# Kernel tuning notes

Measured on AMD Instinct MI355X. Metric: run time of the kernel, lower is better.

## Reference

```python
import jax, jax.numpy as jnp
import numpy as np

EMBED_DIM = 768
NUM_HEADS = 12


def setup_inputs() -> dict:
    key = jax.random.key(0)
    k_x, k_w1, k_b1, k_w2, k_b2 = jax.random.split(key, 5)
    B, S, D = 4, 2048, EMBED_DIM
    s1 = 1.0 / np.sqrt(D)
    return {
        "x": jax.random.normal(k_x, (B, S, D), dtype=jnp.float32),
        "W1": jax.random.uniform(k_w1, (D, 3 * D), jnp.float32, -s1, s1),  # proj1 weight (in,out)
        "b1": jax.random.uniform(k_b1, (3 * D,), jnp.float32, -s1, s1),
        "W2": jax.random.uniform(k_w2, (D, D), jnp.float32, -s1, s1),  # proj2 weight (in,out)
        "b2": jax.random.uniform(k_b2, (D,), jnp.float32, -s1, s1),
    }


def reference(x, W1, b1, W2, b2):
    B, S, D = x.shape
    H = NUM_HEADS
    h = D // H
    qkv = x @ W1 + b1                       # [B,S,3D]
    qkv = qkv.reshape(B, S, H, 3 * h).transpose(0, 2, 1, 3)  # [B,H,S,3h]
    # chunk order in the original: K, Q, V
    K = qkv[..., :h]
    Q = qkv[..., h:2 * h]
    V = qkv[..., 2 * h:]
    # NOTE: original code computes Q @ V^T (not Q @ K^T) -- reproduced faithfully
    scores = jnp.einsum("bhqd,bhkd->bhqk", Q, V) / jnp.sqrt(jnp.float32(h))
    att = jax.nn.softmax(scores, axis=-1)
    out = jnp.einsum("bhqk,bhkd->bhqd", att, V)  # [B,H,S,h]
    out = out.transpose(0, 2, 1, 3).reshape(B, S, D)
    return out @ W2 + b2
```

## Files before the change

### kernel.cpp

```cpp
#include <hip/hip_runtime.h>
#include <hip/hip_bf16.h>
#include <math.h>


#define SEQ   2048
#define DIM   768
#define NHEAD 12
#define HDIM  64
#define BATCH 4

#define QSCALE 0.1803368801111244f

typedef __attribute__((ext_vector_type(8))) short s16x8;
typedef __attribute__((ext_vector_type(4))) float f32x4;

#if __has_builtin(__builtin_amdgcn_exp2f)
#define EXP2F(x) __builtin_amdgcn_exp2f(x)
#else
#define EXP2F(x) exp2f(x)
#endif

__device__ __forceinline__ unsigned short f2bf(float f) {
    union { float f; unsigned int u; } v; v.f = f;
    unsigned int r = v.u + 0x7fffu + ((v.u >> 16) & 1u);
    return (unsigned short)(r >> 16);
}

__device__ __forceinline__ unsigned int cvt_pk_bf16(float a, float b) {
    unsigned int r;
    asm("v_cvt_pk_bf16_f32 %0, %1, %2" : "=v"(r) : "v"(a), "v"(b));
    return r;
}

__device__ __forceinline__ void gload_lds16(const void* g, void* l) {
    __builtin_amdgcn_global_load_lds(
        (const __attribute__((address_space(1))) unsigned int*)g,
        (__attribute__((address_space(3))) unsigned int*)l, 16, 0, 0);
}

__global__ __launch_bounds__(256) void cvt_all(
    const float* __restrict__ x, const float* __restrict__ W1,
    const float* __restrict__ W2, unsigned short* __restrict__ xb,
    unsigned short* __restrict__ W1bt, unsigned short* __restrict__ W2bt)
{
    __shared__ float T[32][33];
    const int id = blockIdx.x;

    if (id >= 1728) {
        const size_t i4 = ((size_t)(id - 1728) * 256 + threadIdx.x) * 4;
        float4 v = *(const float4*)&x[i4];
        ushort4 o;
        o.x = f2bf(v.x); o.y = f2bf(v.y); o.z = f2bf(v.z); o.w = f2bf(v.w);
        *(ushort4*)&xb[i4] = o;
        return;
    }

    const float* W;
    unsigned short* out;
    int n0, k0, src_ld, c0;
    if (id < 1152) {
        W = W1; out = W1bt; src_ld = 2304;
        n0 = (id % 48) * 32; k0 = (id / 48) * 32;
        c0 = (n0 >> 7) * 192 + 64 + (n0 & 127);
    } else {
        const int id2 = id - 1152;
        W = W2; out = W2bt; src_ld = DIM;
        n0 = (id2 % 24) * 32; k0 = (id2 / 24) * 32;
        c0 = n0;
    }
    const int tc = threadIdx.x & 31, tr = threadIdx.x >> 5;
    #pragma unroll
    for (int i = 0; i < 4; ++i)
        T[tr + i * 8][tc] = W[(size_t)(k0 + tr + i * 8) * src_ld + c0 + tc];
    __syncthreads();
    #pragma unroll
    for (int i = 0; i < 4; ++i)
        out[(size_t)(n0 + tr + i * 8) * DIM + k0 + tc] = f2bf(T[tc][tr + i * 8]);
}

__device__ __forceinline__ void gemm128_loop_dbuf(
    const unsigned short* __restrict__ A, const unsigned short* __restrict__ B,
    unsigned short* L, int m0, int n0, f32x4 acc[4][4])
{
    const int tid  = threadIdx.x;
    const int wave = tid >> 6;
    const int lane = tid & 63;
    const int quad = lane >> 4;
    const int lcol = lane & 15;
    const int wm = wave >> 1, wn = wave & 1;

    const int sr = lane >> 2;
    const int sp = lane & 3;
    const int sc = sp ^ ((sr >> 1) & 3);

    const int aswz = ((quad ^ ((lcol >> 1) & 3)) << 4);

    s16x8 ra[2], rb[2];
    #pragma unroll
    for (int s = 0; s < 2; ++s) {
        const int r0 = wave * 32 + s * 16;
        ra[s] = *(const s16x8*)&A[(size_t)(m0 + r0 + sr) * DIM + sc * 8];
        rb[s] = *(const s16x8*)&B[(size_t)(n0 + r0 + sr) * DIM + sc * 8];
    }
    #pragma unroll
    for (int s = 0; s < 2; ++s) {
        const int r0 = wave * 32 + s * 16;
        *(s16x8*)((char*)(L + r0 * 32) + lane * 16) = ra[s];
        *(s16x8*)((char*)(L + 8192 + r0 * 32) + lane * 16) = rb[s];
    }
    __syncthreads();

    int cur = 0;
    for (int k0 = 0; k0 < DIM; k0 += 32) {
        const bool more = (k0 + 32 < DIM);
        if (more) {
            #pragma unroll
            for (int s = 0; s < 2; ++s) {
                const int r0 = wave * 32 + s * 16;
                ra[s] = *(const s16x8*)&A[(size_t)(m0 + r0 + sr) * DIM + k0 + 32 + sc * 8];
                rb[s] = *(const s16x8*)&B[(size_t)(n0 + r0 + sr) * DIM + k0 + 32 + sc * 8];
            }
            __builtin_amdgcn_sched_barrier(0);
        }

        const unsigned short* AsC = L + cur * 4096;
        const unsigned short* BsC = L + 8192 + cur * 4096;

        s16x8 af[4], bf[4];
        #pragma unroll
        for (int mt = 0; mt < 4; ++mt) {
            const int row = wm * 64 + mt * 16 + lcol;
            af[mt] = *(const s16x8*)((const char*)AsC + row * 64 + aswz);
        }
        #pragma unroll
        for (int nt = 0; nt < 4; ++nt) {
            const int row = wn * 64 + nt * 16 + lcol;
            bf[nt] = *(const s16x8*)((const char*)BsC + row * 64 + aswz);
        }
        #pragma unroll
        for (int mt = 0; mt < 4; ++mt)
            #pragma unroll
            for (int nt = 0; nt < 4; ++nt)
                acc[mt][nt] = __builtin_amdgcn_mfma_f32_16x16x32_bf16(
                    af[mt], bf[nt], acc[mt][nt], 0, 0, 0);

        if (more) {
            const int nb = cur ^ 1;
            #pragma unroll
            for (int s = 0; s < 2; ++s) {
                const int r0 = wave * 32 + s * 16;
                *(s16x8*)((char*)(L + nb * 4096 + r0 * 32) + lane * 16) = ra[s];
                *(s16x8*)((char*)(L + 8192 + nb * 4096 + r0 * 32) + lane * 16) = rb[s];
            }
        }
        __syncthreads();
        cur ^= 1;
    }
}

__global__ __launch_bounds__(256) void qkv_gemm_bf16(
    const unsigned short* __restrict__ xb, const unsigned short* __restrict__ W1bt,
    const float* __restrict__ b1, unsigned short* __restrict__ Qb,
    unsigned short* __restrict__ Vr, unsigned short* __restrict__ Vt)
{
    __shared__ unsigned short LDSBUF[16384];
    f32x4 acc[4][4] = {};
    const int id  = blockIdx.y * 12 + blockIdx.x;
    const int swz = (id & 7) * 96 + (id >> 3);
    const int m0 = (swz / 12) * 128, n0 = (swz % 12) * 128;
    gemm128_loop_dbuf(xb, W1bt, LDSBUF, m0, n0, acc);

    const int tid  = threadIdx.x;
    const int wave = tid >> 6, lane = tid & 63;
    const int quad = lane >> 4, lcol = lane & 15;
    const int wm = wave >> 1, wn = wave & 1;

    const int colblock = n0 + wn * 64;
    const int head = colblock >> 7;
    const int cc0  = colblock & 127;
    const int isQ  = (cc0 == 0);
    const float scale = isQ ? QSCALE : 1.0f;
    unsigned short* dst = isQ ? Qb : Vr;

    float bias[4];
    #pragma unroll
    for (int nt = 0; nt < 4; ++nt)
        bias[nt] = b1[head * 192 + 64 + cc0 + nt * 16 + lcol];

    unsigned short* Wst = LDSBUF + wave * 2048;

    #pragma unroll
    for (int half = 0; half < 2; ++half) {
        #pragma unroll
        for (int mh = 0; mh < 2; ++mh) {
            const int mt = half * 2 + mh;
            #pragma unroll
            for (int nt = 0; nt < 4; ++nt)
                #pragma unroll
                for (int r = 0; r < 4; ++r) {
                    const float v = (acc[mt][nt][r] + bias[nt]) * scale;
                    Wst[(mh * 16 + quad * 4 + r) * 64 + nt * 16 + lcol] = f2bf(v);
                }
        }
        __syncthreads();
        #pragma unroll
        for (int p = 0; p < 4; ++p) {
            const int lr = p * 8 + (lane >> 3);
            const int c8 = (lane & 7) * 8;
            s16x8 v = *(const s16x8*)&Wst[lr * 64 + c8];
            const int m  = m0 + wm * 64 + half * 32 + lr;
            const int bb = m >> 11;
            const int s  = m & 2047;
            const int bhh = bb * NHEAD + head;
            *(s16x8*)&dst[((size_t)bhh * SEQ + s) * HDIM + c8] = v;
        }
        __syncthreads();
    }

    if (!isQ) {
        #pragma unroll
        for (int nt = 0; nt < 4; ++nt) {
            const int d = nt * 16 + lcol;
            #pragma unroll
            for (int mt = 0; mt < 4; ++mt) {
                const int m0r = m0 + wm * 64 + mt * 16 + quad * 4;
                const int bb  = m0r >> 11;
                const int s0  = m0r & 2047;
                const int bhh = bb * NHEAD + head;
                ushort4 o;
                o.x = f2bf(acc[mt][nt][0] + bias[nt]);
                o.y = f2bf(acc[mt][nt][1] + bias[nt]);
                o.z = f2bf(acc[mt][nt][2] + bias[nt]);
                o.w = f2bf(acc[mt][nt][3] + bias[nt]);
                *(ushort4*)&Vt[((size_t)bhh * HDIM + d) * SEQ + s0] = o;
            }
        }
    }
}

__global__ __launch_bounds__(256) void attn_mfma(
    const unsigned short* __restrict__ Qb, const unsigned short* __restrict__ Vr,
    const unsigned short* __restrict__ Vt, unsigned short* __restrict__ Yb)
{
    __shared__ unsigned short VrS[2][64 * 64];
    __shared__ unsigned short VtS[2][64 * 64];
    __shared__ unsigned short Ps[4][32 * 72];

    const int bh = blockIdx.x;
    const int b  = bh / NHEAD;
    const int hh = bh % NHEAD;
    const int q0 = blockIdx.y * 128;

    const int tid  = threadIdx.x;
    const int wave = tid >> 6;
    const int lane = tid & 63;
    const int quad = lane >> 4;
    const int lcol = lane & 15;

    s16x8 qa[2][2];
    #pragma unroll
    for (int mt = 0; mt < 2; ++mt)
        #pragma unroll
        for (int kk = 0; kk < 2; ++kk)
            qa[mt][kk] = *(const s16x8*)&Qb[((size_t)bh * SEQ + q0 + wave * 32 + mt * 16 + lcol) * HDIM
                                            + kk * 32 + quad * 8];

    s16x8 ones;
    #pragma unroll
    for (int i = 0; i < 8; ++i) ones[i] = (short)0x3F80;

    f32x4 oacc[2][4] = {};
    f32x4 lsum[2] = {};

    const int srow = lane >> 3;
    const int schk = (lane & 7) ^ srow;

    s16x8 rv[2], rt[2];
    #pragma unroll
    for (int s = 0; s < 2; ++s) {
        const int r0 = wave * 16 + s * 8;
        rv[s] = *(const s16x8*)&Vr[((size_t)bh * SEQ + r0 + srow) * HDIM + schk * 8];
        rt[s] = *(const s16x8*)&Vt[((size_t)bh * HDIM + r0 + srow) * SEQ + schk * 8];
    }
    #pragma unroll
    for (int s = 0; s < 2; ++s) {
        const int r0 = wave * 16 + s * 8;
        *(s16x8*)((char*)&VrS[0][r0 * 64] + lane * 16) = rv[s];
        *(s16x8*)((char*)&VtS[0][r0 * 64] + lane * 16) = rt[s];
    }
    __syncthreads();

    int cur = 0;
    for (int k0 = 0; k0 < SEQ; k0 += 64) {
        const bool more = (k0 + 64 < SEQ);
        if (more) {
            #pragma unroll
            for (int s = 0; s < 2; ++s) {
                const int r0 = wave * 16 + s * 8;
                rv[s] = *(const s16x8*)&Vr[((size_t)bh * SEQ + k0 + 64 + r0 + srow) * HDIM + schk * 8];
                rt[s] = *(const s16x8*)&Vt[((size_t)bh * HDIM + r0 + srow) * SEQ + k0 + 64 + schk * 8];
            }
            __builtin_amdgcn_sched_barrier(0);
        }

        const unsigned short* VrC = &VrS[cur][0];
        const unsigned short* VtC = &VtS[cur][0];

        f32x4 sT[4][2] = {};
        #pragma unroll
        for (int kk = 0; kk < 2; ++kk) {
            s16x8 af[4];
            #pragma unroll
            for (int kt = 0; kt < 4; ++kt) {
                const int r = kt * 16 + lcol;
                const int c = kk * 4 + quad;
                af[kt] = *(const s16x8*)((const char*)VrC + r * 128 + ((c ^ (r & 7)) << 4));
            }
            #pragma unroll
            for (int kt = 0; kt < 4; ++kt)
                #pragma unroll
                for (int mt = 0; mt < 2; ++mt)
                    sT[kt][mt] = __builtin_amdgcn_mfma_f32_16x16x32_bf16(
                        af[kt], qa[mt][kk], sT[kt][mt], 0, 0, 0);
        }

        #pragma unroll
        for (int kt = 0; kt < 4; ++kt)
            #pragma unroll
            for (int mt = 0; mt < 2; ++mt) {
                const float p0 = EXP2F(sT[kt][mt][0]);
                const float p1 = EXP2F(sT[kt][mt][1]);
                const float p2 = EXP2F(sT[kt][mt][2]);
                const float p3 = EXP2F(sT[kt][mt][3]);
                uint2 w;
                w.x = cvt_pk_bf16(p0, p1);
                w.y = cvt_pk_bf16(p2, p3);
                *(uint2*)&Ps[wave][(mt * 16 + lcol) * 72 + kt * 16 + quad * 4] = w;
            }

        #pragma unroll
        for (int kk = 0; kk < 2; ++kk) {
            s16x8 pa[2];
            #pragma unroll
            for (int mt = 0; mt < 2; ++mt)
                pa[mt] = *(const s16x8*)&Ps[wave][(mt * 16 + lcol) * 72 + kk * 32 + quad * 8];
            #pragma unroll
            for (int mt = 0; mt < 2; ++mt)
                lsum[mt] = __builtin_amdgcn_mfma_f32_16x16x32_bf16(
                    pa[mt], ones, lsum[mt], 0, 0, 0);
            #pragma unroll
            for (int dt = 0; dt < 4; ++dt) {
                const int r = dt * 16 + lcol;
                const int c = kk * 4 + quad;
                s16x8 vb = *(const s16x8*)((const char*)VtC + r * 128 + ((c ^ (r & 7)) << 4));
                #pragma unroll
                for (int mt = 0; mt < 2; ++mt)
                    oacc[mt][dt] = __builtin_amdgcn_mfma_f32_16x16x32_bf16(
                        pa[mt], vb, oacc[mt][dt], 0, 0, 0);
            }
        }

        if (more) {
            const int nb = cur ^ 1;
            #pragma unroll
            for (int s = 0; s < 2; ++s) {
                const int r0 = wave * 16 + s * 8;
                *(s16x8*)((char*)&VrS[nb][r0 * 64] + lane * 16) = rv[s];
                *(s16x8*)((char*)&VtS[nb][r0 * 64] + lane * 16) = rt[s];
            }
        }
        __syncthreads();
        cur ^= 1;
    }

    #pragma unroll
    for (int mt = 0; mt < 2; ++mt)
        #pragma unroll
        for (int r = 0; r < 4; ++r) {
            const float invl = 1.0f / lsum[mt][r];
            const int qrow = q0 + wave * 32 + mt * 16 + quad * 4 + r;
            #pragma unroll
            for (int dt = 0; dt < 4; ++dt)
                Yb[((size_t)b * SEQ + qrow) * DIM + hh * HDIM + dt * 16 + lcol] =
                    f2bf(oacc[mt][dt][r] * invl);
        }
}

__global__ __launch_bounds__(256) void proj_gemm_bf16(
    const unsigned short* __restrict__ Yb, const unsigned short* __restrict__ W2bt,
    const float* __restrict__ b2, float* __restrict__ out)
{
    __shared__ unsigned short LDSBUF[8192];
    unsigned short* As = LDSBUF;
    unsigned short* Bs = LDSBUF + 2048;

    const int tid  = threadIdx.x;
    const int wave = tid >> 6;
    const int lane = tid & 63;
    const int quad = lane >> 4;
    const int lcol = lane & 15;
    const int wm = wave >> 1, wn = wave & 1;

    const int id  = blockIdx.y * 6 + blockIdx.x;
    const int swz = (id & 7) * 96 + (id >> 3);
    const int m0 = (swz / 6) * 64, n0 = (swz % 6) * 128;

    const int sr = lane >> 2;
    const int sp = lane & 3;
    const int sc = sp ^ ((sr >> 1) & 3);
    const int aswz = ((quad ^ ((lcol >> 1) & 3)) << 4);

    f32x4 acc[2][4] = {};

    for (int k0 = 0; k0 < DIM; k0 += 32) {
        {
            const int r0 = wave * 16;
            gload_lds16(&Yb[(size_t)(m0 + r0 + sr) * DIM + k0 + sc * 8],
                        (void*)&As[r0 * 32]);
        }
        #pragma unroll
        for (int s = 0; s < 2; ++s) {
            const int r0 = wave * 32 + s * 16;
            gload_lds16(&W2bt[(size_t)(n0 + r0 + sr) * DIM + k0 + sc * 8],
                        (void*)&Bs[r0 * 32]);
        }
        __syncthreads();

        s16x8 af[2], bf[4];
        #pragma unroll
        for (int mt = 0; mt < 2; ++mt) {
            const int row = wm * 32 + mt * 16 + lcol;
            af[mt] = *(const s16x8*)((const char*)As + row * 64 + aswz);
        }
        #pragma unroll
        for (int nt = 0; nt < 4; ++nt) {
            const int row = wn * 64 + nt * 16 + lcol;
            bf[nt] = *(const s16x8*)((const char*)Bs + row * 64 + aswz);
        }
        #pragma unroll
        for (int mt = 0; mt < 2; ++mt)
            #pragma unroll
            for (int nt = 0; nt < 4; ++nt)
                acc[mt][nt] = __builtin_amdgcn_mfma_f32_16x16x32_bf16(
                    af[mt], bf[nt], acc[mt][nt], 0, 0, 0);
        __syncthreads();
    }

    float bias[4];
    #pragma unroll
    for (int nt = 0; nt < 4; ++nt)
        bias[nt] = b2[n0 + wn * 64 + nt * 16 + lcol];

    float* W32 = (float*)LDSBUF + wave * 1024;

    #pragma unroll
    for (int mt = 0; mt < 2; ++mt) {
        #pragma unroll
        for (int nt = 0; nt < 4; ++nt)
            #pragma unroll
            for (int r = 0; r < 4; ++r)
                W32[(quad * 4 + r) * 64 + nt * 16 + lcol] = acc[mt][nt][r] + bias[nt];
        __syncthreads();
        #pragma unroll
        for (int p = 0; p < 4; ++p) {
            const int lr = p * 4 + (lane >> 4);
            float4 v = *(const float4*)&W32[lr * 64 + (lane & 15) * 4];
            const int m = m0 + wm * 32 + mt * 16 + lr;
            *(float4*)&out[(size_t)m * DIM + n0 + wn * 64 + (lane & 15) * 4] = v;
        }
        __syncthreads();
    }
}

extern "C" void kernel_launch(void* const* d_in, const int* in_sizes, int n_in,
                              void* d_out, int out_size, void* d_ws, size_t ws_size,
                              hipStream_t stream)
{
    const float* x  = (const float*)d_in[0];
    const float* W1 = (const float*)d_in[1];
    const float* b1 = (const float*)d_in[2];
    const float* W2 = (const float*)d_in[3];
    const float* b2 = (const float*)d_in[4];
    float* out = (float*)d_out;

    const size_t NQV = (size_t)BATCH * NHEAD * SEQ * HDIM;
    unsigned short* Qb   = (unsigned short*)d_ws;
    unsigned short* Vr   = Qb + NQV;
    unsigned short* Vt   = Vr + NQV;
    unsigned short* Yb   = Vt + NQV;
    unsigned short* xb   = Yb + NQV;
    unsigned short* W1bt = xb + NQV;
    unsigned short* W2bt = W1bt + 1536 * DIM;

    cvt_all<<<7872, 256, 0, stream>>>(x, W1, W2, xb, W1bt, W2bt);

    qkv_gemm_bf16<<<dim3(12, 64), 256, 0, stream>>>(xb, W1bt, b1, Qb, Vr, Vt);
    attn_mfma<<<dim3(BATCH * NHEAD, SEQ / 128), 256, 0, stream>>>(Qb, Vr, Vt, Yb);
    proj_gemm_bf16<<<dim3(DIM / 128, 128), 256, 0, stream>>>(Yb, W2bt, b2, out);
}
```

Measured before the change: 198.9 us.

## Double-buffer output projection GEMM with register-staged global prefetch

```diff
diff --git a/kernel.cpp b/kernel.cpp
--- a/kernel.cpp
+++ b/kernel.cpp
@@ -390,9 +390,8 @@
     const unsigned short* __restrict__ Yb, const unsigned short* __restrict__ W2bt,
     const float* __restrict__ b2, float* __restrict__ out)
 {
-    __shared__ unsigned short LDSBUF[8192];
-    unsigned short* As = LDSBUF;
-    unsigned short* Bs = LDSBUF + 2048;
+    __shared__ unsigned short LDSBUF[12288];
+    unsigned short* const L = LDSBUF;
 
     const int tid  = threadIdx.x;
     const int wave = tid >> 6;
@@ -412,30 +411,51 @@
 
     f32x4 acc[2][4] = {};
 
-    for (int k0 = 0; k0 < DIM; k0 += 32) {
-        {
-            const int r0 = wave * 16;
-            gload_lds16(&Yb[(size_t)(m0 + r0 + sr) * DIM + k0 + sc * 8],
-                        (void*)&As[r0 * 32]);
-        }
+    s16x8 ra, rb[2];
+    {
+        const int r0a = wave * 16;
+        ra = *(const s16x8*)&Yb[(size_t)(m0 + r0a + sr) * DIM + sc * 8];
         #pragma unroll
         for (int s = 0; s < 2; ++s) {
             const int r0 = wave * 32 + s * 16;
-            gload_lds16(&W2bt[(size_t)(n0 + r0 + sr) * DIM + k0 + sc * 8],
-                        (void*)&Bs[r0 * 32]);
-        }
-        __syncthreads();
+            rb[s] = *(const s16x8*)&W2bt[(size_t)(n0 + r0 + sr) * DIM + sc * 8];
+        }
+        *(s16x8*)((char*)(L + r0a * 32) + lane * 16) = ra;
+        #pragma unroll
+        for (int s = 0; s < 2; ++s) {
+            const int r0 = wave * 32 + s * 16;
+            *(s16x8*)((char*)(L + 4096 + r0 * 32) + lane * 16) = rb[s];
+        }
+    }
+    __syncthreads();
+
+    int cur = 0;
+    for (int k0 = 0; k0 < DIM; k0 += 32) {
+        const bool more = (k0 + 32 < DIM);
+        if (more) {
+            const int r0a = wave * 16;
+            ra = *(const s16x8*)&Yb[(size_t)(m0 + r0a + sr) * DIM + k0 + 32 + sc * 8];
+            #pragma unroll
+            for (int s = 0; s < 2; ++s) {
+                const int r0 = wave * 32 + s * 16;
+                rb[s] = *(const s16x8*)&W2bt[(size_t)(n0 + r0 + sr) * DIM + k0 + 32 + sc * 8];
+            }
+            __builtin_amdgcn_sched_barrier(0);
+        }
+
+        const unsigned short* AsC = L + cur * 2048;
+        const unsigned short* BsC = L + 4096 + cur * 4096;
 
         s16x8 af[2], bf[4];
         #pragma unroll
         for (int mt = 0; mt < 2; ++mt) {
             const int row = wm * 32 + mt * 16 + lcol;
-            af[mt] = *(const s16x8*)((const char*)As + row * 64 + aswz);
+            af[mt] = *(const s16x8*)((const char*)AsC + row * 64 + aswz);
         }
         #pragma unroll
         for (int nt = 0; nt < 4; ++nt) {
             const int row = wn * 64 + nt * 16 + lcol;
-            bf[nt] = *(const s16x8*)((const char*)Bs + row * 64 + aswz);
+            bf[nt] = *(const s16x8*)((const char*)BsC + row * 64 + aswz);
         }
         #pragma unroll
         for (int mt = 0; mt < 2; ++mt)
@@ -443,7 +463,19 @@
             for (int nt = 0; nt < 4; ++nt)
                 acc[mt][nt] = __builtin_amdgcn_mfma_f32_16x16x32_bf16(
                     af[mt], bf[nt], acc[mt][nt], 0, 0, 0);
-        __syncthreads();
+
+        if (more) {
+            const int nb = cur ^ 1;
+            const int r0a = wave * 16;
+            *(s16x8*)((char*)(L + nb * 2048 + r0a * 32) + lane * 16) = ra;
+            #pragma unroll
+            for (int s = 0; s < 2; ++s) {
+                const int r0 = wave * 32 + s * 16;
+                *(s16x8*)((char*)(L + 4096 + nb * 4096 + r0 * 32) + lane * 16) = rb[s];
+            }
+        }
+        __syncthreads();
+        cur ^= 1;
     }
 
     float bias[4];
```

Result: no change. 195.7 us (median of 2 runs) (-1.6%).
